# Performance work log

Hardware: AMD Instinct MI355X
Metric: run time of the kernel (lower is better)

Reference implementation:

```python
import jax, jax.numpy as jnp
import numpy as np

CLASS_DIM = 4   # hardcoded in DsFunction1
PROTO_DIM = 20  # hardcoded in DsFunction1


def setup_inputs() -> dict:
    key = jax.random.key(0)
    k1, k2, k3 = jax.random.split(key, 3)
    B, C, H, Wd, D = 2, 16, 64, 64, 64
    inp = jax.random.normal(k1, (B, C, H, Wd, D), dtype=jnp.float32)
    W = jax.random.normal(k2, (PROTO_DIM, C), dtype=jnp.float32)
    BETA = jax.random.normal(k3, (PROTO_DIM, CLASS_DIM), dtype=jnp.float32) * 0.5
    alpha = jnp.zeros((PROTO_DIM, 1), dtype=jnp.float32)           # init 0 per reset_parameters
    gamma = jnp.full((PROTO_DIM, 1), 0.1, dtype=jnp.float32)       # init 0.1 per reset_parameters
    return {"input": inp, "W": W, "BETA": BETA, "alpha": alpha, "gamma": gamma}


def _ds_forward(x, W, BETA, alpha, gamma):
    # x: [B,C,H,Wd,D]; W: [K,C]; BETA: [K,M]; alpha, gamma: [K,1]
    B, C, H, Wd, D = x.shape
    BETA2 = BETA * BETA
    U = BETA2 / jnp.sum(BETA2, axis=1, keepdims=True)              # [K,M] membership weights
    alphap = 0.99 / (1.0 + jnp.exp(-alpha[:, 0]))                  # [K]

    # squared distances to prototypes: d[k] = 0.5 * ||x - W_k||^2 over channel dim
    x2 = jnp.sum(x * x, axis=1)                                    # [B,H,Wd,D]
    xw = jnp.einsum('bchwd,kc->kbhwd', x, W)                       # [K,B,H,Wd,D]
    w2 = jnp.sum(W * W, axis=1)                                    # [K]
    d = 0.5 * (x2[None] - 2.0 * xw + w2[:, None, None, None, None])  # [K,B,H,Wd,D]

    g2 = (gamma[:, 0] ** 2)[:, None, None, None, None]
    s = alphap[:, None, None, None, None] * jnp.exp(-g2 * d)       # [K,B,H,Wd,D]

    mfoc = U[:, :, None, None, None, None] * s[:, None]            # [K,M,B,H,Wd,D] focal masses
    momega = 1.0 - s                                               # [K,B,H,Wd,D] mass on Omega

    # sequential Dempster (unnormalized conjunctive) combination over prototypes
    def step(carry, km):
        mk_f, mk_o = carry                                         # [M,B,H,Wd,D], [B,H,Wd,D]
        m_f, m_o = km
        new_f = mk_f * (m_f + m_o[None]) + m_f * mk_o[None]
        new_o = mk_o * m_o
        return (new_f, new_o), None

    init = (jnp.zeros((CLASS_DIM, B, H, Wd, D), x.dtype),
            jnp.ones((B, H, Wd, D), x.dtype))
    (mk_f, mk_o), _ = jax.lax.scan(step, init, (mfoc, momega))

    mk = jnp.concatenate([mk_f, mk_o[None]], axis=0)               # [M+1,B,H,Wd,D]
    mk_n = mk / jnp.sum(mk, axis=0, keepdims=True)                 # normalize masses
    return jnp.transpose(mk_n, (1, 0, 2, 3, 4))                    # [B,M+1,H,Wd,D]


def reference(input, W, BETA, alpha, gamma):
    return _ds_forward(input, W, BETA, alpha, gamma)
```

## Files before the change

kernel.cpp:

```cpp
#include <hip/hip_runtime.h>
#include <math.h>

#define NK 20
#define NC 16
#define NM 4
#define CSTRIDE 32

__global__ void ds_prep(const float* __restrict__ Wg,
                        const float* __restrict__ BETAg,
                        const float* __restrict__ alphag,
                        const float* __restrict__ gammag,
                        float* __restrict__ ws)
{
    const int k = threadIdx.x;
    if (k >= NK) return;
    const float L   = 1.4426950408889634f;
    const float g   = gammag[k];
    const float g2L = g * g * L;
    float w2 = 0.f;
    #pragma unroll
    for (int c = 0; c < NC; ++c) {
        const float w = Wg[k*NC + c];
        ws[k*CSTRIDE + c] = g2L * w;
        w2 = fmaf(w, w, w2);
    }
    const float a = 0.99f / (1.0f + __expf(-alphag[k]));
    ws[k*CSTRIDE + 16] = -0.5f * g2L;
    ws[k*CSTRIDE + 17] = -0.5f * g2L * w2;
    float b0 = BETAg[k*NM+0], b1 = BETAg[k*NM+1], b2 = BETAg[k*NM+2], b3 = BETAg[k*NM+3];
    b0 *= b0; b1 *= b1; b2 *= b2; b3 *= b3;
    const float uinv = 1.0f / (b0 + b1 + b2 + b3);
    ws[k*CSTRIDE + 18] = (1.0f - b0 * uinv) * a;
    ws[k*CSTRIDE + 19] = (1.0f - b1 * uinv) * a;
    ws[k*CSTRIDE + 20] = (1.0f - b2 * uinv) * a;
    ws[k*CSTRIDE + 21] = (1.0f - b3 * uinv) * a;
    ws[k*CSTRIDE + 22] = a;
}

__global__ __launch_bounds__(256, 4) void ds_main(
    const float* __restrict__ inp,
    const float* __restrict__ cw,
    float* __restrict__ out,
    int S2,
    int total2)
{
    const int i2 = blockIdx.x * 256 + threadIdx.x;
    if (i2 >= total2) return;

    const int S  = S2 * 2;
    const int b  = (i2 >= S2) ? 1 : 0;
    const int sp = (i2 - b * S2) * 2;

    const float* xb = inp + (size_t)b * NC * S + sp;
    float x[NC][2];
    float x2[2] = {0.f, 0.f};
    #pragma unroll
    for (int c = 0; c < NC; ++c) {
        const float2 v = *(const float2*)(xb + (size_t)c * S);
        x[c][0] = v.x; x[c][1] = v.y;
        x2[0] = fmaf(v.x, v.x, x2[0]);
        x2[1] = fmaf(v.y, v.y, x2[1]);
    }

    float P[NM+1][2];
    #pragma unroll
    for (int m = 0; m <= NM; ++m) { P[m][0] = 1.f; P[m][1] = 1.f; }

    #pragma unroll 4
    for (int k = 0; k < NK; ++k) {
        const float* row = cw + k * CSTRIDE;
        const float nh = row[16], nbk = row[17];
        float dp0 = fmaf(nh, x2[0], nbk);
        float dp1 = fmaf(nh, x2[1], nbk);
        #pragma unroll
        for (int c = 0; c < NC; ++c) {
            const float w = row[c];
            dp0 = fmaf(x[c][0], w, dp0);
            dp1 = fmaf(x[c][1], w, dp1);
        }
        const float e0 = __builtin_amdgcn_exp2f(dp0);
        const float e1 = __builtin_amdgcn_exp2f(dp1);
        #pragma unroll
        for (int m = 0; m <= NM; ++m) {
            const float cm = row[18 + m];
            P[m][0] *= fmaf(-cm, e0, 1.0f);
            P[m][1] *= fmaf(-cm, e1, 1.0f);
        }
    }

    float* ob = out + (size_t)b * (NM+1) * S + sp;
    float r[NM+1][2];
    #pragma unroll
    for (int j = 0; j < 2; ++j) {
        const float O  = P[NM][j];
        const float f0 = P[0][j] - O, f1 = P[1][j] - O,
                    f2 = P[2][j] - O, f3 = P[3][j] - O;
        const float tot = f0 + f1 + f2 + f3 + O;
        const float inv = 1.0f / tot;
        r[0][j] = f0 * inv;
        r[1][j] = f1 * inv;
        r[2][j] = f2 * inv;
        r[3][j] = f3 * inv;
        r[4][j] = O  * inv;
    }
    #pragma unroll
    for (int m = 0; m <= NM; ++m) {
        *(float2*)(ob + (size_t)m * S) = make_float2(r[m][0], r[m][1]);
    }
}

extern "C" void kernel_launch(void* const* d_in, const int* in_sizes, int n_in,
                              void* d_out, int out_size, void* d_ws, size_t ws_size,
                              hipStream_t stream) {
    const float* inp   = (const float*)d_in[0];
    const float* Wg    = (const float*)d_in[1];
    const float* BETAg = (const float*)d_in[2];
    const float* alphag= (const float*)d_in[3];
    const float* gammag= (const float*)d_in[4];
    float* out = (float*)d_out;
    float* ws  = (float*)d_ws;

    const int BS     = in_sizes[0] / NC;
    const int B      = 2;
    const int S      = BS / B;
    const int S2     = S / 2;
    const int total2 = BS / 2;

    ds_prep<<<1, 64, 0, stream>>>(Wg, BETAg, alphag, gammag, ws);

    const int block = 256;
    const int grid  = (total2 + block - 1) / block;
    ds_main<<<grid, block, 0, stream>>>(inp, ws, out, S2, total2);
}
```

Before: 90.22 us.

## Compute prototype distances with bf16 MFMA instead of scalar FMAs

The prototype distance dot products now run as a 32x32x16 bf16 MFMA, with a second MFMA folding in the squared-norm and bias terms. Each wave handles tiles of 32 spatial points, and each half-wave owns half of the prototype rows. The two halves combine their partial Dempster products with cross-lane shuffles, and only one half stores the result. The prep kernel now packs the scaled W and bias terms as bf16, padded to 32 rows. This removes most of the scalar FMA work per point, at the cost of bf16 rounding of inputs inside an exponent and redundant exp work on padded rows.

```diff
diff --git a/kernel.cpp b/kernel.cpp
--- a/kernel.cpp
+++ b/kernel.cpp
@@ -1,10 +1,19 @@
 #include <hip/hip_runtime.h>
+#include <hip/hip_bf16.h>
 #include <math.h>
 
 #define NK 20
 #define NC 16
 #define NM 4
-#define CSTRIDE 32
+#define TSTEP 4
+
+typedef __attribute__((ext_vector_type(8)))  short  short8;
+typedef __attribute__((ext_vector_type(16))) float  floatx16;
+
+static __device__ __forceinline__ short bf16b(float f) {
+    __hip_bfloat16 h = __float2bfloat16(f);
+    return *reinterpret_cast<short*>(&h);
+}
 
 __global__ void ds_prep(const float* __restrict__ Wg,
                         const float* __restrict__ BETAg,
@@ -12,100 +21,131 @@
                         const float* __restrict__ gammag,
                         float* __restrict__ ws)
 {
-    const int k = threadIdx.x;
-    if (k >= NK) return;
-    const float L   = 1.4426950408889634f;
-    const float g   = gammag[k];
-    const float g2L = g * g * L;
-    float w2 = 0.f;
-    #pragma unroll
-    for (int c = 0; c < NC; ++c) {
-        const float w = Wg[k*NC + c];
-        ws[k*CSTRIDE + c] = g2L * w;
-        w2 = fmaf(w, w, w2);
+    const int p = threadIdx.x;
+    if (p >= 32) return;
+    float* cst = ws;
+    short* Wpb = (short*)(ws + 256);
+    short* A2b = (short*)(ws + 512);
+    if (p < NK) {
+        const float L   = 1.4426950408889634f;
+        const float g   = gammag[p];
+        const float g2L = g * g * L;
+        float w2 = 0.f;
+        #pragma unroll
+        for (int c = 0; c < NC; ++c) {
+            const float w = Wg[p*NC + c];
+            Wpb[p*NC + c] = bf16b(g2L * w);
+            w2 = fmaf(w, w, w2);
+        }
+        const float a = 0.99f / (1.0f + __expf(-alphag[p]));
+        float b0 = BETAg[p*NM+0], b1 = BETAg[p*NM+1], b2 = BETAg[p*NM+2], b3 = BETAg[p*NM+3];
+        b0 *= b0; b1 *= b1; b2 *= b2; b3 *= b3;
+        const float uinv = 1.0f / (b0 + b1 + b2 + b3);
+        cst[p*8+0] = (1.0f - b0*uinv) * a;
+        cst[p*8+1] = (1.0f - b1*uinv) * a;
+        cst[p*8+2] = (1.0f - b2*uinv) * a;
+        cst[p*8+3] = (1.0f - b3*uinv) * a;
+        cst[p*8+4] = a;
+        cst[p*8+5] = 0.f; cst[p*8+6] = 0.f; cst[p*8+7] = 0.f;
+        A2b[p*2+0] = bf16b(-0.5f * g2L);
+        A2b[p*2+1] = bf16b(-0.5f * g2L * w2);
+    } else {
+        #pragma unroll
+        for (int i = 0; i < 8; ++i) cst[p*8+i] = 0.f;
+        #pragma unroll
+        for (int c = 0; c < NC; ++c) Wpb[p*NC + c] = 0;
+        A2b[p*2+0] = 0; A2b[p*2+1] = 0;
     }
-    const float a = 0.99f / (1.0f + __expf(-alphag[k]));
-    ws[k*CSTRIDE + 16] = -0.5f * g2L;
-    ws[k*CSTRIDE + 17] = -0.5f * g2L * w2;
-    float b0 = BETAg[k*NM+0], b1 = BETAg[k*NM+1], b2 = BETAg[k*NM+2], b3 = BETAg[k*NM+3];
-    b0 *= b0; b1 *= b1; b2 *= b2; b3 *= b3;
-    const float uinv = 1.0f / (b0 + b1 + b2 + b3);
-    ws[k*CSTRIDE + 18] = (1.0f - b0 * uinv) * a;
-    ws[k*CSTRIDE + 19] = (1.0f - b1 * uinv) * a;
-    ws[k*CSTRIDE + 20] = (1.0f - b2 * uinv) * a;
-    ws[k*CSTRIDE + 21] = (1.0f - b3 * uinv) * a;
-    ws[k*CSTRIDE + 22] = a;
 }
 
 __global__ __launch_bounds__(256, 4) void ds_main(
     const float* __restrict__ inp,
-    const float* __restrict__ cw,
+    const float* __restrict__ ws,
     float* __restrict__ out,
-    int S2,
-    int total2)
+    int S,
+    int BS)
 {
-    const int i2 = blockIdx.x * 256 + threadIdx.x;
-    if (i2 >= total2) return;
+    const int lane = threadIdx.x & 63;
+    const int half = lane >> 5;
+    const int col  = lane & 31;
+    const int gw   = blockIdx.x * 4 + (threadIdx.x >> 6);
 
-    const int S  = S2 * 2;
-    const int b  = (i2 >= S2) ? 1 : 0;
-    const int sp = (i2 - b * S2) * 2;
+    const float* cst = ws;
+    const short* Wpb = (const short*)(ws + 256);
+    const short* A2b = (const short*)(ws + 512);
 
-    const float* xb = inp + (size_t)b * NC * S + sp;
-    float x[NC][2];
-    float x2[2] = {0.f, 0.f};
+    const short8 afrag = *(const short8*)(Wpb + col*NC + half*8);
+    short8 a2frag;
     #pragma unroll
-    for (int c = 0; c < NC; ++c) {
-        const float2 v = *(const float2*)(xb + (size_t)c * S);
-        x[c][0] = v.x; x[c][1] = v.y;
-        x2[0] = fmaf(v.x, v.x, x2[0]);
-        x2[1] = fmaf(v.y, v.y, x2[1]);
+    for (int j = 0; j < 8; ++j) a2frag[j] = 0;
+    if (half == 0) { a2frag[0] = A2b[col*2+0]; a2frag[1] = A2b[col*2+1]; }
+
+    float cm0[12], cm1[12], cm2[12], cm3[12], cO[12];
+    #pragma unroll
+    for (int r = 0; r < 12; ++r) {
+        const int p = (r & 3) + 8*(r >> 2) + 4*half;
+        const float4 cv = *(const float4*)(cst + p*8);
+        cm0[r] = cv.x; cm1[r] = cv.y; cm2[r] = cv.z; cm3[r] = cv.w;
+        cO[r]  = cst[p*8 + 4];
     }
 
-    float P[NM+1][2];
     #pragma unroll
-    for (int m = 0; m <= NM; ++m) { P[m][0] = 1.f; P[m][1] = 1.f; }
+    for (int t = 0; t < TSTEP; ++t) {
+        const int base = (gw * TSTEP + t) * 32;
+        if (base >= BS) break;
+        const int e  = base + col;
+        const int b  = (e >= S) ? 1 : 0;
+        const int sp = e - b * S;
+        const float* xb = inp + (size_t)b * NC * S + sp;
 
-    #pragma unroll 4
-    for (int k = 0; k < NK; ++k) {
-        const float* row = cw + k * CSTRIDE;
-        const float nh = row[16], nbk = row[17];
-        float dp0 = fmaf(nh, x2[0], nbk);
-        float dp1 = fmaf(nh, x2[1], nbk);
+        short8 bfrag;
+        float x2p = 0.f;
         #pragma unroll
-        for (int c = 0; c < NC; ++c) {
-            const float w = row[c];
-            dp0 = fmaf(x[c][0], w, dp0);
-            dp1 = fmaf(x[c][1], w, dp1);
+        for (int j = 0; j < 8; ++j) {
+            const float v = xb[(size_t)(8*half + j) * S];
+            x2p = fmaf(v, v, x2p);
+            bfrag[j] = bf16b(v);
         }
-        const float e0 = __builtin_amdgcn_exp2f(dp0);
-        const float e1 = __builtin_amdgcn_exp2f(dp1);
+        const float x2 = x2p + __shfl_xor(x2p, 32, 64);
+
+        short8 b2frag;
         #pragma unroll
-        for (int m = 0; m <= NM; ++m) {
-            const float cm = row[18 + m];
-            P[m][0] *= fmaf(-cm, e0, 1.0f);
-            P[m][1] *= fmaf(-cm, e1, 1.0f);
+        for (int j = 0; j < 8; ++j) b2frag[j] = 0;
+        if (half == 0) { b2frag[0] = bf16b(x2); b2frag[1] = (short)0x3F80; }
+
+        floatx16 acc;
+        #pragma unroll
+        for (int i = 0; i < 16; ++i) acc[i] = 0.f;
+        acc = __builtin_amdgcn_mfma_f32_32x32x16_bf16(afrag,  bfrag,  acc, 0, 0, 0);
+        acc = __builtin_amdgcn_mfma_f32_32x32x16_bf16(a2frag, b2frag, acc, 0, 0, 0);
+
+        float P0 = 1.f, P1 = 1.f, P2 = 1.f, P3 = 1.f, PO = 1.f;
+        #pragma unroll
+        for (int r = 0; r < 12; ++r) {
+            const float ek = __builtin_amdgcn_exp2f(acc[r]);
+            P0 *= fmaf(-cm0[r], ek, 1.0f);
+            P1 *= fmaf(-cm1[r], ek, 1.0f);
+            P2 *= fmaf(-cm2[r], ek, 1.0f);
+            P3 *= fmaf(-cm3[r], ek, 1.0f);
+            PO *= fmaf(-cO[r],  ek, 1.0f);
         }
-    }
+        P0 *= __shfl_xor(P0, 32, 64);
+        P1 *= __shfl_xor(P1, 32, 64);
+        P2 *= __shfl_xor(P2, 32, 64);
+        P3 *= __shfl_xor(P3, 32, 64);
+        PO *= __shfl_xor(PO, 32, 64);
 
-    float* ob = out + (size_t)b * (NM+1) * S + sp;
-    float r[NM+1][2];
-    #pragma unroll
-    for (int j = 0; j < 2; ++j) {
-        const float O  = P[NM][j];
-        const float f0 = P[0][j] - O, f1 = P[1][j] - O,
-                    f2 = P[2][j] - O, f3 = P[3][j] - O;
-        const float tot = f0 + f1 + f2 + f3 + O;
-        const float inv = 1.0f / tot;
-        r[0][j] = f0 * inv;
-        r[1][j] = f1 * inv;
-        r[2][j] = f2 * inv;
-        r[3][j] = f3 * inv;
-        r[4][j] = O  * inv;
-    }
-    #pragma unroll
-    for (int m = 0; m <= NM; ++m) {
-        *(float2*)(ob + (size_t)m * S) = make_float2(r[m][0], r[m][1]);
+        const float O  = PO;
+        const float f0 = P0 - O, f1 = P1 - O, f2 = P2 - O, f3 = P3 - O;
+        const float inv = 1.0f / (f0 + f1 + f2 + f3 + O);
+        if (half == 0) {
+            float* op = out + (size_t)b * (NM+1) * S + sp;
+            op[0]            = f0 * inv;
+            op[(size_t)S]    = f1 * inv;
+            op[(size_t)2*S]  = f2 * inv;
+            op[(size_t)3*S]  = f3 * inv;
+            op[(size_t)4*S]  = O  * inv;
+        }
     }
 }
 
@@ -120,15 +160,12 @@
     float* out = (float*)d_out;
     float* ws  = (float*)d_ws;
 
-    const int BS     = in_sizes[0] / NC;
-    const int B      = 2;
-    const int S      = BS / B;
-    const int S2     = S / 2;
-    const int total2 = BS / 2;
+    const int BS = in_sizes[0] / NC;
+    const int S  = BS / 2;
 
     ds_prep<<<1, 64, 0, stream>>>(Wg, BETAg, alphag, gammag, ws);
 
-    const int block = 256;
-    const int grid  = (total2 + block - 1) / block;
-    ds_main<<<grid, block, 0, stream>>>(inp, ws, out, S2, total2);
+    const int elems_per_block = 4 * TSTEP * 32;
+    const int grid = (BS + elems_per_block - 1) / elems_per_block;
+    ds_main<<<grid, 256, 0, stream>>>(inp, ws, out, S, BS);
 }
```

After: 86.47 us. 4.2% less time.
